# Kernel optimization log

Hardware: AMD Instinct MI355X
Metric: run time of the kernel (lower is better)

Reference implementation:

```python
import jax, jax.numpy as jnp
import numpy as np
from jax import lax

K = 12          # filterbank order (units per group)
G = 2           # number of groups / filterbanks
T_SAMP = 1.0    # samp_interval
B, S = 2048, 2048


def setup_inputs() -> dict:
    key = jax.random.key(0)
    k1, k2 = jax.random.split(key)
    x = jax.random.normal(k1, (B, S, G), dtype=jnp.float32)
    # relax in (0.2, 0.8) so sqrt(relax) and sqrt(1-relax) are well-behaved
    relax = 0.2 + 0.6 * jax.random.uniform(k2, (G,), dtype=jnp.float32)
    return {"x": x, "relax": relax}


def reference(x, relax):
    """Laguerre FilterbankCell unrolled over time with lax.scan.

    x:     [B, S, G] input sequence (one channel per filterbank group)
    relax: [G]       per-group relaxation parameter in (0,1)
    returns [B, S, G, K] filterbank outputs per timestep.
    """
    sa = jnp.sqrt(relax)            # sqrt(relax_i),    [G]
    sb = jnp.sqrt(1.0 - relax)      # sqrt(1-relax_i),  [G]

    def step(prev, xt):
        # prev: [B, G, K] previous filterbank state; xt: [B, G]
        y0 = sa[None, :] * prev[:, :, 0] + T_SAMP * sb[None, :] * xt  # [B, G]
        ys = [y0]
        for j in range(1, K):  # K is small and fixed -> unrolled lag chain
            yj = sa[None, :] * prev[:, :, j] + sa[None, :] * ys[-1] - prev[:, :, j - 1]
            ys.append(yj)
        y = jnp.stack(ys, axis=2)  # [B, G, K]
        return y, y

    init = jnp.zeros((x.shape[0], G, K), dtype=x.dtype)
    xs = jnp.moveaxis(x, 1, 0)                 # [S, B, G]
    _, outs = lax.scan(step, init, xs)         # [S, B, G, K]
    return jnp.moveaxis(outs, 0, 1)            # [B, S, G, K]
```

## Files before the change

### kernel.cpp

```cpp
#include <hip/hip_runtime.h>


#define KF 12
#define GF 2
#define BF 2048
#define SF 2048
#define BG (BF * GF)
#define PSTR 52

__device__ __forceinline__ void fb_step2(float* __restrict__ y0, float* __restrict__ y1,
                                         float x0, float x1,
                                         float sa0, float tsb0, float sa1, float tsb1) {
    float pm0 = y0[0], pm1 = y1[0];
    y0[0] = fmaf(sa0, y0[0], tsb0 * x0);
    y1[0] = fmaf(sa1, y1[0], tsb1 * x1);
    #pragma unroll
    for (int j = 1; j < KF; ++j) {
        const float t0 = y0[j], t1 = y1[j];
        y0[j] = fmaf(sa0, t0, fmaf(sa0, y0[j - 1], -pm0));
        y1[j] = fmaf(sa1, t1, fmaf(sa1, y1[j - 1], -pm1));
        pm0 = t0; pm1 = t1;
    }
}

template <int NC>
__global__ void setup_mpow(const float* __restrict__ relax, float* __restrict__ Mp) {
    constexpr int LCH = SF / NC;
    constexpr int LOG2L = (LCH == 16) ? 4 : ((LCH == 32) ? 5 : 6);
    const int g = blockIdx.x;
    const int t = threadIdx.x;
    __shared__ float A[KF][KF];
    const float rx = relax[g];
    const float sa = sqrtf(rx);

    if (t < KF * KF) {
        const int j = t / KF, m = t % KF;
        float v = 0.0f;
        if (m == j) {
            v = sa;
        } else if (m < j) {
            float p = 1.0f;
            for (int i = 0; i < j - m - 1; ++i) p *= sa;
            v = -(1.0f - rx) * p;
        }
        A[j][m] = v;
    }
    __syncthreads();

    for (int it = 0; it < LOG2L; ++it) {
        float s = 0.0f;
        if (t < KF * KF) {
            const int j = t / KF, m = t % KF;
            #pragma unroll
            for (int i = 0; i < KF; ++i) s += A[j][i] * A[i][m];
        }
        __syncthreads();
        if (t < KF * KF) A[t / KF][t % KF] = s;
        __syncthreads();
    }

    if (t < KF * KF) Mp[g * KF * KF + t] = A[t / KF][t % KF];
}

template <int NC>
__global__ __launch_bounds__(256, 4) void pass1_chunk_states(
        const float* __restrict__ x, const float* __restrict__ relax,
        float* __restrict__ F) {
    constexpr int LCH = SF / NC;
    const int tid = blockIdx.x * 256 + threadIdx.x;
    const int c = tid & (NC - 1);
    const int b = tid / NC;

    const float r0 = relax[0], r1 = relax[1];
    const float sa0 = sqrtf(r0), tsb0 = sqrtf(1.0f - r0);
    const float sa1 = sqrtf(r1), tsb1 = sqrtf(1.0f - r1);

    float y0[KF], y1[KF];
    #pragma unroll
    for (int k = 0; k < KF; ++k) { y0[k] = 0.0f; y1[k] = 0.0f; }

    const float4* xp = (const float4*)(x + ((size_t)b * SF + (size_t)c * LCH) * GF);
    for (int t2 = 0; t2 < LCH / 2; ++t2) {
        const float4 xv = xp[t2];
        fb_step2(y0, y1, xv.x, xv.y, sa0, tsb0, sa1, tsb1);
        fb_step2(y0, y1, xv.z, xv.w, sa0, tsb0, sa1, tsb1);
    }

    float4* Fp = (float4*)(F + ((size_t)b * NC + c) * (GF * KF));
    Fp[0] = make_float4(y0[0], y0[1], y0[2],  y0[3]);
    Fp[1] = make_float4(y0[4], y0[5], y0[6],  y0[7]);
    Fp[2] = make_float4(y0[8], y0[9], y0[10], y0[11]);
    Fp[3] = make_float4(y1[0], y1[1], y1[2],  y1[3]);
    Fp[4] = make_float4(y1[4], y1[5], y1[6],  y1[7]);
    Fp[5] = make_float4(y1[8], y1[9], y1[10], y1[11]);
}

template <int NC>
__global__ void pass2_combine(float* __restrict__ F, const float* __restrict__ Mp) {
    const int tid = blockIdx.x * blockDim.x + threadIdx.x;
    const int sub = tid & 15;
    const int bg  = tid >> 4;
    const int b   = bg >> 1;
    const int g   = bg & 1;
    const int lane = threadIdx.x & 63;
    const int grpbase = lane & ~15;

    const int k = (sub < KF) ? sub : 0;
    float Mrow[KF];
    const float* mr = Mp + ((size_t)g * KF + k) * KF;
    #pragma unroll
    for (int m = 0; m < KF; ++m) Mrow[m] = mr[m];

    float* Fb = F + ((size_t)b * NC) * (GF * KF) + g * KF + k;

    float r = 0.0f;
    float fnext = Fb[0];
    for (int c = 1; c < NC; ++c) {
        const float fcur = fnext;
        if (c + 1 < NC) fnext = Fb[(size_t)c * (GF * KF)];
        float acc = fcur;
        #pragma unroll
        for (int m = 0; m < KF; ++m) {
            acc += Mrow[m] * __shfl(r, grpbase + m, 64);
        }
        if (sub < KF) Fb[(size_t)(c - 1) * (GF * KF)] = acc;
        r = acc;
    }
}

template <int NC>
__global__ __launch_bounds__(256, 3) void pass3_outputs(
        const float* __restrict__ x, const float* __restrict__ relax,
        const float* __restrict__ F, float* __restrict__ out) {
    constexpr int LCH = SF / NC;
    constexpr int WPB = NC / 64;
    __shared__ __align__(16) float lds[4 * 64 * PSTR];

    const int lane = threadIdx.x & 63;
    const int w    = threadIdx.x >> 6;
    const int W    = blockIdx.x * 4 + w;
    const int b    = W / WPB;
    const int c0   = (W % WPB) * 64;
    const int c    = c0 + lane;

    const float r0 = relax[0], r1 = relax[1];
    const float sa0 = sqrtf(r0), tsb0 = sqrtf(1.0f - r0);
    const float sa1 = sqrtf(r1), tsb1 = sqrtf(1.0f - r1);

    float y0[KF], y1[KF];
    if (c == 0) {
        #pragma unroll
        for (int k = 0; k < KF; ++k) { y0[k] = 0.0f; y1[k] = 0.0f; }
    } else {
        const float4* Fp = (const float4*)(F + ((size_t)b * NC + (c - 1)) * (GF * KF));
        const float4 a0 = Fp[0], a1 = Fp[1], a2 = Fp[2];
        const float4 a3 = Fp[3], a4 = Fp[4], a5 = Fp[5];
        y0[0] = a0.x; y0[1] = a0.y; y0[2]  = a0.z; y0[3]  = a0.w;
        y0[4] = a1.x; y0[5] = a1.y; y0[6]  = a1.z; y0[7]  = a1.w;
        y0[8] = a2.x; y0[9] = a2.y; y0[10] = a2.z; y0[11] = a2.w;
        y1[0] = a3.x; y1[1] = a3.y; y1[2]  = a3.z; y1[3]  = a3.w;
        y1[4] = a4.x; y1[5] = a4.y; y1[6]  = a4.z; y1[7]  = a4.w;
        y1[8] = a5.x; y1[9] = a5.y; y1[10] = a5.z; y1[11] = a5.w;
    }

    const float4* xp = (const float4*)(x + ((size_t)b * SF + (size_t)c * LCH) * GF);

    float* Lw  = lds + (size_t)w * 64 * PSTR;
    float* Lme = Lw + lane * PSTR;

    const float4* Lrd[12];
    int goff[12];
    #pragma unroll
    for (int j = 0; j < 12; ++j) {
        const int v = j * 64 + lane;
        const int p = v / 12;
        const int f = v - p * 12;
        Lrd[j]  = (const float4*)(Lw + p * PSTR + f * 4);
        goff[j] = (c0 + p) * (LCH * 6) + f;
    }
    float4* outb = (float4*)(out + (size_t)b * SF * (GF * KF));

    for (int i = 0; i < LCH / 2; ++i) {
        const float4 xv = xp[i];

        fb_step2(y0, y1, xv.x, xv.y, sa0, tsb0, sa1, tsb1);
        float4* Ls = (float4*)Lme;
        Ls[0] = make_float4(y0[0], y0[1], y0[2],  y0[3]);
        Ls[1] = make_float4(y0[4], y0[5], y0[6],  y0[7]);
        Ls[2] = make_float4(y0[8], y0[9], y0[10], y0[11]);
        Ls[3] = make_float4(y1[0], y1[1], y1[2],  y1[3]);
        Ls[4] = make_float4(y1[4], y1[5], y1[6],  y1[7]);
        Ls[5] = make_float4(y1[8], y1[9], y1[10], y1[11]);

        fb_step2(y0, y1, xv.z, xv.w, sa0, tsb0, sa1, tsb1);
        Ls[6]  = make_float4(y0[0], y0[1], y0[2],  y0[3]);
        Ls[7]  = make_float4(y0[4], y0[5], y0[6],  y0[7]);
        Ls[8]  = make_float4(y0[8], y0[9], y0[10], y0[11]);
        Ls[9]  = make_float4(y1[0], y1[1], y1[2],  y1[3]);
        Ls[10] = make_float4(y1[4], y1[5], y1[6],  y1[7]);
        Ls[11] = make_float4(y1[8], y1[9], y1[10], y1[11]);

        const int tbase = 12 * i;
        #pragma unroll
        for (int j = 0; j < 12; ++j) {
            outb[(size_t)(goff[j] + tbase)] = *Lrd[j];
        }
    }
}

template <int NC>
static void run_all(const float* x, const float* relax, float* out,
                    float* Mp, float* F, hipStream_t stream) {
    setup_mpow<NC><<<GF, 192, 0, stream>>>(relax, Mp);
    const int threads13 = BF * NC;
    pass1_chunk_states<NC><<<threads13 / 256, 256, 0, stream>>>(x, relax, F);
    pass2_combine<NC><<<(BG * 16) / 256, 256, 0, stream>>>(F, Mp);
    pass3_outputs<NC><<<threads13 / 256, 256, 0, stream>>>(x, relax, F, out);
}

extern "C" void kernel_launch(void* const* d_in, const int* in_sizes, int n_in,
                              void* d_out, int out_size, void* d_ws, size_t ws_size,
                              hipStream_t stream) {
    const float* x     = (const float*)d_in[0];
    const float* relax = (const float*)d_in[1];
    float* out = (float*)d_out;

    float* Mp = (float*)d_ws;
    float* F  = (float*)((char*)d_ws + 4096);

    const size_t need128 = 4096 + (size_t)BF * 128 * (GF * KF) * sizeof(float);
    if (ws_size >= need128) {
        run_all<128>(x, relax, out, Mp, F, stream);
    } else {
        run_all<64>(x, relax, out, Mp, F, stream);
    }
}
```

Before: 534.7 us.

## Stage four timesteps per window with XOR-swizzled LDS and 128-thread blocks

The output pass now runs four filter steps per window before flushing, staging 24 float4s per lane into LDS with an XOR swizzle instead of a padded stride. Each lane then issues 24 wider coalesced global stores per window (384 contiguous bytes per chunk row). Blocks shrink to two wavefronts with per-wave LDS of 24KB, which changes occupancy. The goal is longer contiguous write bursts and fewer LDS bank conflicts, at the cost of more registers for the 24 offset pairs and more LDS per wave.

```diff
diff --git a/kernel.cpp b/kernel.cpp
--- a/kernel.cpp
+++ b/kernel.cpp
@@ -6,7 +6,6 @@
 #define BF 2048
 #define SF 2048
 #define BG (BF * GF)
-#define PSTR 52
 
 __device__ __forceinline__ void fb_step2(float* __restrict__ y0, float* __restrict__ y1,
                                          float x0, float x1,
@@ -128,17 +127,30 @@
     }
 }
 
-template <int NC>
-__global__ __launch_bounds__(256, 3) void pass3_outputs(
+__device__ __forceinline__ void stage24(char* Lw, int kbase, int sswz,
+                                        const float* __restrict__ y0,
+                                        const float* __restrict__ y1) {
+    *(float4*)(Lw + ((kbase +  0) ^ sswz)) = make_float4(y0[0], y0[1], y0[2],  y0[3]);
+    *(float4*)(Lw + ((kbase + 16) ^ sswz)) = make_float4(y0[4], y0[5], y0[6],  y0[7]);
+    *(float4*)(Lw + ((kbase + 32) ^ sswz)) = make_float4(y0[8], y0[9], y0[10], y0[11]);
+    *(float4*)(Lw + ((kbase + 48) ^ sswz)) = make_float4(y1[0], y1[1], y1[2],  y1[3]);
+    *(float4*)(Lw + ((kbase + 64) ^ sswz)) = make_float4(y1[4], y1[5], y1[6],  y1[7]);
+    *(float4*)(Lw + ((kbase + 80) ^ sswz)) = make_float4(y1[8], y1[9], y1[10], y1[11]);
+}
+
+template <int NC>
+__global__ __launch_bounds__(128) void pass3_outputs(
         const float* __restrict__ x, const float* __restrict__ relax,
         const float* __restrict__ F, float* __restrict__ out) {
-    constexpr int LCH = SF / NC;
-    constexpr int WPB = NC / 64;
-    __shared__ __align__(16) float lds[4 * 64 * PSTR];
+    constexpr int LCH   = SF / NC;
+    constexpr int WPB   = NC / 64;
+    constexpr int NWIN  = LCH / 4;
+    constexpr int ROWF4 = LCH * 6;
+    __shared__ __align__(16) float lds[2 * 64 * 96];
 
     const int lane = threadIdx.x & 63;
     const int w    = threadIdx.x >> 6;
-    const int W    = blockIdx.x * 4 + w;
+    const int W    = blockIdx.x * 2 + w;
     const int b    = W / WPB;
     const int c0   = (W % WPB) * 64;
     const int c    = c0 + lane;
@@ -163,47 +175,40 @@
         y1[8] = a5.x; y1[9] = a5.y; y1[10] = a5.z; y1[11] = a5.w;
     }
 
+    char* Lw = (char*)&lds[w * 64 * 96];
+    const int sbase = lane * 384;
+    const int sswz  = (lane & 7) << 4;
+
+    int gof[24], lof[24];
+    #pragma unroll
+    for (int j = 0; j < 24; ++j) {
+        const int v  = j * 64 + lane;
+        const int cf = v / 24;
+        const int qf = v - cf * 24;
+        gof[j] = (c0 + cf) * ROWF4 + qf;
+        lof[j] = (cf * 384 + qf * 16) ^ ((cf & 7) << 4);
+    }
+
     const float4* xp = (const float4*)(x + ((size_t)b * SF + (size_t)c * LCH) * GF);
-
-    float* Lw  = lds + (size_t)w * 64 * PSTR;
-    float* Lme = Lw + lane * PSTR;
-
-    const float4* Lrd[12];
-    int goff[12];
-    #pragma unroll
-    for (int j = 0; j < 12; ++j) {
-        const int v = j * 64 + lane;
-        const int p = v / 12;
-        const int f = v - p * 12;
-        Lrd[j]  = (const float4*)(Lw + p * PSTR + f * 4);
-        goff[j] = (c0 + p) * (LCH * 6) + f;
-    }
     float4* outb = (float4*)(out + (size_t)b * SF * (GF * KF));
 
-    for (int i = 0; i < LCH / 2; ++i) {
-        const float4 xv = xp[i];
-
-        fb_step2(y0, y1, xv.x, xv.y, sa0, tsb0, sa1, tsb1);
-        float4* Ls = (float4*)Lme;
-        Ls[0] = make_float4(y0[0], y0[1], y0[2],  y0[3]);
-        Ls[1] = make_float4(y0[4], y0[5], y0[6],  y0[7]);
-        Ls[2] = make_float4(y0[8], y0[9], y0[10], y0[11]);
-        Ls[3] = make_float4(y1[0], y1[1], y1[2],  y1[3]);
-        Ls[4] = make_float4(y1[4], y1[5], y1[6],  y1[7]);
-        Ls[5] = make_float4(y1[8], y1[9], y1[10], y1[11]);
-
-        fb_step2(y0, y1, xv.z, xv.w, sa0, tsb0, sa1, tsb1);
-        Ls[6]  = make_float4(y0[0], y0[1], y0[2],  y0[3]);
-        Ls[7]  = make_float4(y0[4], y0[5], y0[6],  y0[7]);
-        Ls[8]  = make_float4(y0[8], y0[9], y0[10], y0[11]);
-        Ls[9]  = make_float4(y1[0], y1[1], y1[2],  y1[3]);
-        Ls[10] = make_float4(y1[4], y1[5], y1[6],  y1[7]);
-        Ls[11] = make_float4(y1[8], y1[9], y1[10], y1[11]);
-
-        const int tbase = 12 * i;
+    for (int win = 0; win < NWIN; ++win) {
+        const float4 xa = xp[2 * win];
+        const float4 xb = xp[2 * win + 1];
+
+        fb_step2(y0, y1, xa.x, xa.y, sa0, tsb0, sa1, tsb1);
+        stage24(Lw, sbase +   0, sswz, y0, y1);
+        fb_step2(y0, y1, xa.z, xa.w, sa0, tsb0, sa1, tsb1);
+        stage24(Lw, sbase +  96, sswz, y0, y1);
+        fb_step2(y0, y1, xb.x, xb.y, sa0, tsb0, sa1, tsb1);
+        stage24(Lw, sbase + 192, sswz, y0, y1);
+        fb_step2(y0, y1, xb.z, xb.w, sa0, tsb0, sa1, tsb1);
+        stage24(Lw, sbase + 288, sswz, y0, y1);
+
+        const int tof = win * 24;
         #pragma unroll
-        for (int j = 0; j < 12; ++j) {
-            outb[(size_t)(goff[j] + tbase)] = *Lrd[j];
+        for (int j = 0; j < 24; ++j) {
+            outb[(size_t)(gof[j] + tof)] = *(const float4*)(Lw + lof[j]);
         }
     }
 }
@@ -212,10 +217,9 @@
 static void run_all(const float* x, const float* relax, float* out,
                     float* Mp, float* F, hipStream_t stream) {
     setup_mpow<NC><<<GF, 192, 0, stream>>>(relax, Mp);
-    const int threads13 = BF * NC;
-    pass1_chunk_states<NC><<<threads13 / 256, 256, 0, stream>>>(x, relax, F);
+    pass1_chunk_states<NC><<<(BF * NC) / 256, 256, 0, stream>>>(x, relax, F);
     pass2_combine<NC><<<(BG * 16) / 256, 256, 0, stream>>>(F, Mp);
-    pass3_outputs<NC><<<threads13 / 256, 256, 0, stream>>>(x, relax, F, out);
+    pass3_outputs<NC><<<(BF * (NC / 64)) / 2, 128, 0, stream>>>(x, relax, F, out);
 }
 
 extern "C" void kernel_launch(void* const* d_in, const int* in_sizes, int n_in,
```

New measurement: 488.2 us. 8.7% less time.
